# Kernel tuning notes

Hardware: AMD Instinct MI355X
Metric: run time of the kernel (lower is better)

## Reference

```python
import jax, jax.numpy as jnp
import numpy as np

N_NODES = 50000
N_EDGES = 600000
D_IN = 128
DIM = 128
N_REL = 3
N_LAYERS = 2


def setup_inputs() -> dict:
    key = jax.random.key(0)
    ks = jax.random.split(key, 10)
    s = 1.0 / np.sqrt(DIM)
    x = jax.random.normal(ks[0], (N_NODES, D_IN), dtype=jnp.float32)
    edge_index = jax.random.randint(ks[1], (2, N_EDGES), 0, N_NODES)
    edge_type = jax.random.randint(ks[2], (N_EDGES,), 0, N_REL)
    edge_weight = jax.random.uniform(ks[3], (N_EDGES,), dtype=jnp.float32)
    # stacked per-layer parameters (layer dims are uniform since D_IN == DIM)
    w_rel = jax.random.normal(ks[4], (N_LAYERS, N_REL, DIM, DIM), dtype=jnp.float32) * s
    w_root = jax.random.normal(ks[5], (N_LAYERS, DIM, DIM), dtype=jnp.float32) * s
    b_conv = jnp.zeros((N_LAYERS, DIM), dtype=jnp.float32)
    w_skip = jax.random.normal(ks[6], (N_LAYERS, D_IN, DIM), dtype=jnp.float32) * s
    b_skip = jnp.zeros((N_LAYERS, DIM), dtype=jnp.float32)
    return {"x": x, "edge_index": edge_index, "edge_type": edge_type,
            "edge_weight": edge_weight, "w_rel": w_rel, "w_root": w_root,
            "b_conv": b_conv, "w_skip": w_skip, "b_skip": b_skip}


def reference(x, edge_index, edge_type, edge_weight, w_rel, w_root, b_conv, w_skip, b_skip):
    n = x.shape[0]
    src, dst = edge_index[0], edge_index[1]
    h = x
    for l in range(w_rel.shape[0]):  # small fixed layer loop (2)
        skip = x @ w_skip[l] + b_skip[l]                      # [N, dim]
        # per-relation transform of all nodes: [R, N, dim] (cheap GEMMs),
        # avoids materializing a per-edge [E, d, d] weight gather
        hr = jnp.einsum('nd,rde->rne', h, w_rel[l])
        msgs = hr[edge_type, src] * edge_weight[:, None]      # [E, dim] gather
        agg = jax.ops.segment_sum(msgs, dst, num_segments=n)  # scatter-add
        h = agg + h @ w_root[l] + b_conv[l] + skip            # conv + skip residual
    return h
```

## Files before the change

kernel.cpp:

```cpp
#include <hip/hip_runtime.h>


#define DIM 128

typedef short short8 __attribute__((ext_vector_type(8)));
typedef float f32x4 __attribute__((ext_vector_type(4)));

__device__ __forceinline__ unsigned short f2bf(float f) {
    unsigned u = __float_as_uint(f);
    unsigned r = (u + 0x7FFFu + ((u >> 16) & 1u)) >> 16;
    return (unsigned short)r;
}
__device__ __forceinline__ float bflo(unsigned p) { return __uint_as_float(p << 16); }
__device__ __forceinline__ float bfhi(unsigned p) { return __uint_as_float(p & 0xFFFF0000u); }

__global__ void zero_kernel(int4* __restrict__ p, int n4) {
    int i = blockIdx.x * 256 + threadIdx.x;
    if (i < n4) p[i] = make_int4(0, 0, 0, 0);
}

#define K2_CONVB 2048
#define K2_PREPB 256
#define K2_CNTB  512

__device__ void conv_body(const float* __restrict__ in, unsigned short* __restrict__ ob,
                          int n8, int bid) {
    for (int i = bid * 256 + threadIdx.x; i < n8; i += K2_CONVB * 256) {
        const float4* ip = reinterpret_cast<const float4*>(in) + (size_t)i * 2;
        float4 v0 = ip[0], v1 = ip[1];
        uint4 o;
        o.x = (unsigned)f2bf(v0.x) | ((unsigned)f2bf(v0.y) << 16);
        o.y = (unsigned)f2bf(v0.z) | ((unsigned)f2bf(v0.w) << 16);
        o.z = (unsigned)f2bf(v1.x) | ((unsigned)f2bf(v1.y) << 16);
        o.w = (unsigned)f2bf(v1.z) | ((unsigned)f2bf(v1.w) << 16);
        reinterpret_cast<uint4*>(ob)[i] = o;
    }
}

__device__ void prep_body(const float* __restrict__ w_rel, const float* __restrict__ w_root,
                          const float* __restrict__ w_skip, unsigned short* __restrict__ WTf,
                          int bid) {
    for (int i = bid * 256 + threadIdx.x; i < 2 * 5 * DIM * DIM; i += K2_PREPB * 256) {
        int j    = i & 7;
        int lane = (i >> 3) & 63;
        int ks   = (i >> 9) & 3;
        int n    = (i >> 11) & 7;
        int s    = (i >> 14) % 5;
        int l    = i / (5 * DIM * DIM);
        int col = n * 16 + (lane & 15);
        int k   = ks * 32 + (lane >> 4) * 8 + j;
        float v;
        if (s < 3)       v = w_rel[(((size_t)l * 3 + s) * DIM + k) * DIM + col];
        else if (s == 3) {
            v = w_root[((size_t)l * DIM + k) * DIM + col];
            if (l == 0) v += w_skip[((size_t)k) * DIM + col];
        } else           v = w_skip[((size_t)l * DIM + k) * DIM + col];
        WTf[i] = f2bf(v);
    }
}

__device__ void count_body(const int* __restrict__ dst, int* __restrict__ counts,
                           unsigned short* __restrict__ rank, int E, int bid) {
    for (int i = bid * 256 + threadIdx.x; i < E; i += K2_CNTB * 256) {
        int r = atomicAdd(&counts[dst[i]], 1);
        rank[i] = (unsigned short)r;
    }
}

__global__ __launch_bounds__(256) void fat_prep(
    const float* __restrict__ x, unsigned short* __restrict__ xb, int n8,
    const float* __restrict__ w_rel, const float* __restrict__ w_root,
    const float* __restrict__ w_skip, unsigned short* __restrict__ WTf,
    const int* __restrict__ dst, int* __restrict__ counts,
    unsigned short* __restrict__ rank, int E) {
    int b = blockIdx.x;
    if (b < K2_CONVB)                 conv_body(x, xb, n8, b);
    else if (b < K2_CONVB + K2_PREPB) prep_body(w_rel, w_root, w_skip, WTf, b - K2_CONVB);
    else                              count_body(dst, counts, rank, E, b - K2_CONVB - K2_PREPB);
}

__global__ void bsum_kernel(const int* __restrict__ counts, int* __restrict__ bsums, int n) {
    int t = threadIdx.x;
    int i = blockIdx.x * 256 + t;
    int v = (i < n) ? counts[i] : 0;
    for (int d = 32; d; d >>= 1) v += __shfl_down(v, d);
    __shared__ int ws[4];
    if ((t & 63) == 0) ws[t >> 6] = v;
    __syncthreads();
    if (t == 0) bsums[blockIdx.x] = ws[0] + ws[1] + ws[2] + ws[3];
}

__global__ void bscan_kernel(const int* __restrict__ bsums, int* __restrict__ bpre, int nblk) {
    __shared__ int s[256];
    int t = threadIdx.x;
    int v = (t < nblk) ? bsums[t] : 0;
    s[t] = v;
    __syncthreads();
    for (int d = 1; d < 256; d <<= 1) {
        int u = (t >= d) ? s[t - d] : 0;
        __syncthreads();
        s[t] += u;
        __syncthreads();
    }
    bpre[t] = s[t] - v;
}

__global__ void scan_final(const int* __restrict__ counts, const int* __restrict__ bpre,
                           int* __restrict__ offsets, int n, int E) {
    __shared__ int s[256];
    int t = threadIdx.x;
    int i = blockIdx.x * 256 + t;
    int v = (i < n) ? counts[i] : 0;
    s[t] = v;
    __syncthreads();
    for (int d = 1; d < 256; d <<= 1) {
        int u = (t >= d) ? s[t - d] : 0;
        __syncthreads();
        s[t] += u;
        __syncthreads();
    }
    int ex = s[t] - v + bpre[blockIdx.x];
    if (i < n) offsets[i] = ex;
    if (i == 0) offsets[n] = E;
}

template<bool HAS_SKIP>
__device__ void gemm_body(
    int bid,
    const unsigned short* __restrict__ Ab, const unsigned short* __restrict__ Xb,
    const unsigned short* __restrict__ WTf,
    const float* __restrict__ bconv, const float* __restrict__ bskip,
    unsigned short* __restrict__ hr, void* __restrict__ outp, int M) {
    constexpr int NF = HAS_SKIP ? 40 : 32;
    __shared__ unsigned short stile[4][32][136];
    int t = threadIdx.x, lane = t & 63, wid = t >> 6;
    int lrow = lane & 15, lhi = lane >> 4;
    int r0 = bid * 128 + wid * 32;

    short8 af[2][4];
    #pragma unroll
    for (int rg = 0; rg < 2; ++rg) {
        int r = r0 + rg * 16 + lrow;
        const unsigned short* ap = Ab + (size_t)(r < M ? r : 0) * DIM + lhi * 8;
        #pragma unroll
        for (int ks = 0; ks < 4; ++ks)
            af[rg][ks] = *reinterpret_cast<const short8*>(ap + ks * 32);
    }
    short8 xf[2][4];
    f32x4 acc34[2][8];

    auto flush = [&](unsigned short* gbase) {
        #pragma unroll
        for (int j = 0; j < 8; ++j) {
            int lr = j * 4 + lhi;
            int lc = lrow * 8;
            int gr = r0 + lr;
            if (gr < M)
                *reinterpret_cast<uint4*>(gbase + (size_t)gr * DIM + lc) =
                    *reinterpret_cast<const uint4*>(&stile[wid][lr][lc]);
        }
    };

    short8 b0[4], b1[4];
    auto loadB = [&](int fi, short8* bb) {
        const unsigned short* p = WTf + ((size_t)fi * 4 * 64 + lane) * 8;
        #pragma unroll
        for (int ks = 0; ks < 4; ++ks)
            bb[ks] = *reinterpret_cast<const short8*>(p + ks * 512);
    };
    loadB(0, b0);
    #pragma unroll
    for (int fi = 0; fi < NF; ++fi) {
        short8* bc = (fi & 1) ? b1 : b0;
        short8* bn = (fi & 1) ? b0 : b1;
        if (fi + 1 < NF) loadB(fi + 1, bn);
        const int slot = fi >> 3, n = fi & 7;
        const int col = n * 16 + lrow;
        if (HAS_SKIP && slot == 3 && n == 0) {
            #pragma unroll
            for (int rg = 0; rg < 2; ++rg) {
                int r = r0 + rg * 16 + lrow;
                const unsigned short* xp = Xb + (size_t)(r < M ? r : 0) * DIM + lhi * 8;
                #pragma unroll
                for (int ks = 0; ks < 4; ++ks)
                    xf[rg][ks] = *reinterpret_cast<const short8*>(xp + ks * 32);
            }
        }
        if (slot < 3) {
            f32x4 a0 = {0.f, 0.f, 0.f, 0.f}, a1 = {0.f, 0.f, 0.f, 0.f};
            #pragma unroll
            for (int ks = 0; ks < 4; ++ks) {
                a0 = __builtin_amdgcn_mfma_f32_16x16x32_bf16(af[0][ks], bc[ks], a0, 0, 0, 0);
                a1 = __builtin_amdgcn_mfma_f32_16x16x32_bf16(af[1][ks], bc[ks], a1, 0, 0, 0);
            }
            #pragma unroll
            for (int rg = 0; rg < 2; ++rg) {
                f32x4& aa = rg ? a1 : a0;
                #pragma unroll
                for (int i2 = 0; i2 < 4; ++i2)
                    stile[wid][rg * 16 + lhi * 4 + i2][col] = f2bf(aa[i2]);
            }
            if (n == 7) flush(hr + (size_t)slot * M * DIM);
        } else if (!HAS_SKIP) {
            f32x4 a0 = {0.f, 0.f, 0.f, 0.f}, a1 = {0.f, 0.f, 0.f, 0.f};
            #pragma unroll
            for (int ks = 0; ks < 4; ++ks) {
                a0 = __builtin_amdgcn_mfma_f32_16x16x32_bf16(af[0][ks], bc[ks], a0, 0, 0, 0);
                a1 = __builtin_amdgcn_mfma_f32_16x16x32_bf16(af[1][ks], bc[ks], a1, 0, 0, 0);
            }
            float bb = bconv[col] + bskip[col];
            #pragma unroll
            for (int rg = 0; rg < 2; ++rg) {
                f32x4& aa = rg ? a1 : a0;
                #pragma unroll
                for (int i2 = 0; i2 < 4; ++i2)
                    stile[wid][rg * 16 + lhi * 4 + i2][col] = f2bf(aa[i2] + bb);
            }
            if (n == 7) flush((unsigned short*)outp);
        } else if (slot == 3) {
            f32x4 z = {0.f, 0.f, 0.f, 0.f};
            acc34[0][n] = z; acc34[1][n] = z;
            #pragma unroll
            for (int ks = 0; ks < 4; ++ks) {
                acc34[0][n] = __builtin_amdgcn_mfma_f32_16x16x32_bf16(af[0][ks], bc[ks], acc34[0][n], 0, 0, 0);
                acc34[1][n] = __builtin_amdgcn_mfma_f32_16x16x32_bf16(af[1][ks], bc[ks], acc34[1][n], 0, 0, 0);
            }
        } else {
            #pragma unroll
            for (int ks = 0; ks < 4; ++ks) {
                acc34[0][n] = __builtin_amdgcn_mfma_f32_16x16x32_bf16(xf[0][ks], bc[ks], acc34[0][n], 0, 0, 0);
                acc34[1][n] = __builtin_amdgcn_mfma_f32_16x16x32_bf16(xf[1][ks], bc[ks], acc34[1][n], 0, 0, 0);
            }
            float bb = bconv[col] + bskip[col];
            float* op = (float*)outp;
            #pragma unroll
            for (int rg = 0; rg < 2; ++rg) {
                #pragma unroll
                for (int i2 = 0; i2 < 4; ++i2) {
                    int r = r0 + rg * 16 + lhi * 4 + i2;
                    if (r < M) op[(size_t)r * DIM + col] = acc34[rg][n][i2] + bb;
                }
            }
        }
    }
}

#define K6_SCTB 512

__device__ void scatter_body(const int* __restrict__ src, const int* __restrict__ dst,
                             const int* __restrict__ etype, const float* __restrict__ ew,
                             const int* __restrict__ offsets,
                             const unsigned short* __restrict__ rank,
                             unsigned* __restrict__ csr, int E, int bid) {
    for (int i = bid * 256 + threadIdx.x; i < E; i += K6_SCTB * 256) {
        int d = dst[i];
        int p = offsets[d] + rank[i];
        unsigned wq = (unsigned)__float2uint_rn(ew[i] * 16383.0f);
        csr[p] = (unsigned)src[i] | ((unsigned)etype[i] << 16) | (wq << 18);
    }
}

__global__ __launch_bounds__(256) void gemm0_scatter(
    const unsigned short* __restrict__ Ab, const unsigned short* __restrict__ WTf,
    const float* __restrict__ bconv, const float* __restrict__ bskip,
    unsigned short* __restrict__ hr, unsigned short* __restrict__ h1, int M, int GB,
    const int* __restrict__ src, const int* __restrict__ dst,
    const int* __restrict__ etype, const float* __restrict__ ew,
    const int* __restrict__ offsets, const unsigned short* __restrict__ rank,
    unsigned* __restrict__ csr, int E) {
    int b = blockIdx.x;
    if (b < GB) gemm_body<false>(b, Ab, nullptr, WTf, bconv, bskip, hr, h1, M);
    else        scatter_body(src, dst, etype, ew, offsets, rank, csr, E, b - GB);
}

__global__ __launch_bounds__(256) void gemm1_kernel(
    const unsigned short* __restrict__ Ab, const unsigned short* __restrict__ Xb,
    const unsigned short* __restrict__ WTf,
    const float* __restrict__ bconv, const float* __restrict__ bskip,
    unsigned short* __restrict__ hr, float* __restrict__ outp, int M) {
    gemm_body<true>(blockIdx.x, Ab, Xb, WTf, bconv, bskip, hr, outp, M);
}

template<bool BF16IO>
__global__ __launch_bounds__(256) void agg_kernel(
    const unsigned short* __restrict__ hr, const unsigned* __restrict__ csr,
    const int* __restrict__ offsets, float* __restrict__ outf,
    unsigned short* __restrict__ outb, int N) {
    int t = threadIdx.x;
    int lane = t & 63;
    int v = blockIdx.x * 4 + (t >> 6);
    if (v >= N) return;
    int g = lane >> 4;
    int l16 = lane & 15;
    int beg = offsets[v], end = offsets[v + 1];

    float acc[8] = {0.f, 0.f, 0.f, 0.f, 0.f, 0.f, 0.f, 0.f};
    int i = beg + g;
    bool valid = i < end;
    unsigned st = valid ? csr[i] : 0u;
    while (__any(valid)) {
        int ni = i + 4;
        bool nv = ni < end;
        unsigned nst = nv ? csr[ni] : 0u;
        if (valid) {
            int srcn = st & 0xFFFF;
            int rel  = (st >> 16) & 3;
            float w  = (float)(st >> 18) * (1.0f / 16383.0f);
            const unsigned short* row = hr + ((size_t)rel * N + srcn) * DIM + l16 * 8;
            uint4 pv = *reinterpret_cast<const uint4*>(row);
            acc[0] += w * bflo(pv.x); acc[1] += w * bfhi(pv.x);
            acc[2] += w * bflo(pv.y); acc[3] += w * bfhi(pv.y);
            acc[4] += w * bflo(pv.z); acc[5] += w * bfhi(pv.z);
            acc[6] += w * bflo(pv.w); acc[7] += w * bfhi(pv.w);
        }
        i = ni; st = nst; valid = nv;
    }
    #pragma unroll
    for (int j = 0; j < 8; ++j) {
        acc[j] += __shfl_xor(acc[j], 16);
        acc[j] += __shfl_xor(acc[j], 32);
    }
    if (g == 0) {
        if (BF16IO) {
            unsigned short* op = outb + (size_t)v * DIM + l16 * 8;
            uint4 cur = *reinterpret_cast<const uint4*>(op);
            float r0 = bflo(cur.x) + acc[0], r1 = bfhi(cur.x) + acc[1];
            float r2 = bflo(cur.y) + acc[2], r3 = bfhi(cur.y) + acc[3];
            float r4 = bflo(cur.z) + acc[4], r5 = bfhi(cur.z) + acc[5];
            float r6 = bflo(cur.w) + acc[6], r7 = bfhi(cur.w) + acc[7];
            uint4 o;
            o.x = (unsigned)f2bf(r0) | ((unsigned)f2bf(r1) << 16);
            o.y = (unsigned)f2bf(r2) | ((unsigned)f2bf(r3) << 16);
            o.z = (unsigned)f2bf(r4) | ((unsigned)f2bf(r5) << 16);
            o.w = (unsigned)f2bf(r6) | ((unsigned)f2bf(r7) << 16);
            *reinterpret_cast<uint4*>(op) = o;
        } else {
            float* op = outf + (size_t)v * DIM + l16 * 8;
            float4 c0 = *reinterpret_cast<float4*>(op);
            float4 c1 = *reinterpret_cast<float4*>(op + 4);
            c0.x += acc[0]; c0.y += acc[1]; c0.z += acc[2]; c0.w += acc[3];
            c1.x += acc[4]; c1.y += acc[5]; c1.z += acc[6]; c1.w += acc[7];
            *reinterpret_cast<float4*>(op) = c0;
            *reinterpret_cast<float4*>(op + 4) = c1;
        }
    }
}

extern "C" void kernel_launch(void* const* d_in, const int* in_sizes, int n_in,
                              void* d_out, int out_size, void* d_ws, size_t ws_size,
                              hipStream_t stream) {
    const float* x       = (const float*)d_in[0];
    const int*   eidx    = (const int*)d_in[1];
    const int*   etype   = (const int*)d_in[2];
    const float* ew      = (const float*)d_in[3];
    const float* w_rel   = (const float*)d_in[4];
    const float* w_root  = (const float*)d_in[5];
    const float* b_conv  = (const float*)d_in[6];
    const float* w_skip  = (const float*)d_in[7];
    const float* b_skip  = (const float*)d_in[8];

    const int N = in_sizes[0] / DIM;
    const int E = in_sizes[3];
    const int* src = eidx;
    const int* dst = eidx + E;
    const int nblk = (N + 255) / 256;

    char* w = (char*)d_ws;
    unsigned short* WTf  = (unsigned short*)w;  w += (size_t)2 * 5 * DIM * DIM * 2;
    unsigned short* xb   = (unsigned short*)w;  w += (size_t)N * DIM * 2;
    unsigned short* hr   = (unsigned short*)w;  w += (size_t)3 * N * DIM * 2;
    unsigned short* h1   = (unsigned short*)w;  w += (size_t)N * DIM * 2;
    int* counts          = (int*)w;             w += (size_t)N * 4;
    int* offsets         = (int*)w;             w += (size_t)(N + 4) * 4;
    int* bsums           = (int*)w;             w += (size_t)256 * 4;
    int* bpre            = (int*)w;             w += (size_t)256 * 4;
    unsigned short* rank = (unsigned short*)w;  w += (size_t)E * 2;
    unsigned* csr        = (unsigned*)w;        w += (size_t)E * 4;

    float* out = (float*)d_out;

    const int n8 = N * DIM / 8;
    zero_kernel<<<(N / 4 + 255) / 256, 256, 0, stream>>>((int4*)counts, N / 4);
    fat_prep<<<K2_CONVB + K2_PREPB + K2_CNTB, 256, 0, stream>>>(
        x, xb, n8, w_rel, w_root, w_skip, WTf, dst, counts, rank, E);
    bsum_kernel<<<nblk, 256, 0, stream>>>(counts, bsums, N);
    bscan_kernel<<<1, 256, 0, stream>>>(bsums, bpre, nblk);
    scan_final<<<nblk, 256, 0, stream>>>(counts, bpre, offsets, N, E);

    int GB = (N + 127) / 128;
    int ablocks = (N + 3) / 4;
    gemm0_scatter<<<GB + K6_SCTB, 256, 0, stream>>>(
        xb, WTf, b_conv, b_skip, hr, h1, N, GB,
        src, dst, etype, ew, offsets, rank, csr, E);
    agg_kernel<true><<<ablocks, 256, 0, stream>>>(hr, csr, offsets, nullptr, h1, N);
    gemm1_kernel<<<GB, 256, 0, stream>>>(h1, xb, WTf + (size_t)5 * DIM * DIM,
                                         b_conv + DIM, b_skip + DIM, hr, out, N);
    agg_kernel<false><<<ablocks, 256, 0, stream>>>(hr, csr, offsets, out, nullptr, N);
}
```

Measured before the change: 159.4 us.

## Privatize degree counters into eight partitions to reduce atomic contention

The per-destination degree counting now spreads its atomics across eight copies of the count array, selected by block index, and each thread issues four independent atomics per iteration for more memory-level parallelism. The scan kernels sum the eight partitions and write per-partition starting positions, which the scatter uses with the edge's partition, recovered from its index, to place CSR entries. This aims to cut same-address atomic contention in the counting phase. In exchange it adds eight times the counter zeroing, extra reads in both scans, and a larger pos0 lookup table in the scatter.

```diff
diff --git a/kernel.cpp b/kernel.cpp
--- a/kernel.cpp
+++ b/kernel.cpp
@@ -59,11 +59,24 @@
     }
 }
 
-__device__ void count_body(const int* __restrict__ dst, int* __restrict__ counts,
-                           unsigned short* __restrict__ rank, int E, int bid) {
-    for (int i = bid * 256 + threadIdx.x; i < E; i += K2_CNTB * 256) {
-        int r = atomicAdd(&counts[dst[i]], 1);
-        rank[i] = (unsigned short)r;
+__device__ void count_body(const int* __restrict__ dst, int* __restrict__ counts8,
+                           unsigned short* __restrict__ rank, int E, int N, int bid) {
+    int* cp = counts8 + (size_t)(bid & 7) * N;
+    int t = threadIdx.x;
+    for (int base = bid * 1024; base < E; base += K2_CNTB * 1024) {
+        int i0 = base + t, i1 = i0 + 256, i2 = i0 + 512, i3 = i0 + 768;
+        int d0 = (i0 < E) ? dst[i0] : -1;
+        int d1 = (i1 < E) ? dst[i1] : -1;
+        int d2 = (i2 < E) ? dst[i2] : -1;
+        int d3 = (i3 < E) ? dst[i3] : -1;
+        int r0 = (d0 >= 0) ? atomicAdd(&cp[d0], 1) : 0;
+        int r1 = (d1 >= 0) ? atomicAdd(&cp[d1], 1) : 0;
+        int r2 = (d2 >= 0) ? atomicAdd(&cp[d2], 1) : 0;
+        int r3 = (d3 >= 0) ? atomicAdd(&cp[d3], 1) : 0;
+        if (d0 >= 0) rank[i0] = (unsigned short)r0;
+        if (d1 >= 0) rank[i1] = (unsigned short)r1;
+        if (d2 >= 0) rank[i2] = (unsigned short)r2;
+        if (d3 >= 0) rank[i3] = (unsigned short)r3;
     }
 }
 
@@ -71,18 +84,22 @@
     const float* __restrict__ x, unsigned short* __restrict__ xb, int n8,
     const float* __restrict__ w_rel, const float* __restrict__ w_root,
     const float* __restrict__ w_skip, unsigned short* __restrict__ WTf,
-    const int* __restrict__ dst, int* __restrict__ counts,
-    unsigned short* __restrict__ rank, int E) {
+    const int* __restrict__ dst, int* __restrict__ counts8,
+    unsigned short* __restrict__ rank, int E, int N) {
     int b = blockIdx.x;
     if (b < K2_CONVB)                 conv_body(x, xb, n8, b);
     else if (b < K2_CONVB + K2_PREPB) prep_body(w_rel, w_root, w_skip, WTf, b - K2_CONVB);
-    else                              count_body(dst, counts, rank, E, b - K2_CONVB - K2_PREPB);
-}
-
-__global__ void bsum_kernel(const int* __restrict__ counts, int* __restrict__ bsums, int n) {
+    else                              count_body(dst, counts8, rank, E, N, b - K2_CONVB - K2_PREPB);
+}
+
+__global__ void bsum_kernel(const int* __restrict__ counts8, int* __restrict__ bsums, int n) {
     int t = threadIdx.x;
     int i = blockIdx.x * 256 + t;
-    int v = (i < n) ? counts[i] : 0;
+    int v = 0;
+    if (i < n) {
+        #pragma unroll
+        for (int p = 0; p < 8; ++p) v += counts8[(size_t)p * n + i];
+    }
     for (int d = 32; d; d >>= 1) v += __shfl_down(v, d);
     __shared__ int ws[4];
     if ((t & 63) == 0) ws[t >> 6] = v;
@@ -105,12 +122,18 @@
     bpre[t] = s[t] - v;
 }
 
-__global__ void scan_final(const int* __restrict__ counts, const int* __restrict__ bpre,
-                           int* __restrict__ offsets, int n, int E) {
+__global__ void scan_final(const int* __restrict__ counts8, const int* __restrict__ bpre,
+                           int* __restrict__ offsets, int* __restrict__ pos0,
+                           int n, int E) {
     __shared__ int s[256];
     int t = threadIdx.x;
     int i = blockIdx.x * 256 + t;
-    int v = (i < n) ? counts[i] : 0;
+    int c[8];
+    int v = 0;
+    if (i < n) {
+        #pragma unroll
+        for (int p = 0; p < 8; ++p) { c[p] = counts8[(size_t)p * n + i]; v += c[p]; }
+    }
     s[t] = v;
     __syncthreads();
     for (int d = 1; d < 256; d <<= 1) {
@@ -120,7 +143,12 @@
         __syncthreads();
     }
     int ex = s[t] - v + bpre[blockIdx.x];
-    if (i < n) offsets[i] = ex;
+    if (i < n) {
+        offsets[i] = ex;
+        int run = ex;
+        #pragma unroll
+        for (int p = 0; p < 8; ++p) { pos0[(size_t)p * n + i] = run; run += c[p]; }
+    }
     if (i == 0) offsets[n] = E;
 }
 
@@ -249,12 +277,13 @@
 
 __device__ void scatter_body(const int* __restrict__ src, const int* __restrict__ dst,
                              const int* __restrict__ etype, const float* __restrict__ ew,
-                             const int* __restrict__ offsets,
+                             const int* __restrict__ pos0,
                              const unsigned short* __restrict__ rank,
-                             unsigned* __restrict__ csr, int E, int bid) {
+                             unsigned* __restrict__ csr, int E, int N, int bid) {
     for (int i = bid * 256 + threadIdx.x; i < E; i += K6_SCTB * 256) {
         int d = dst[i];
-        int p = offsets[d] + rank[i];
+        int part = (i >> 10) & 7;
+        int p = pos0[(size_t)part * N + d] + rank[i];
         unsigned wq = (unsigned)__float2uint_rn(ew[i] * 16383.0f);
         csr[p] = (unsigned)src[i] | ((unsigned)etype[i] << 16) | (wq << 18);
     }
@@ -266,11 +295,11 @@
     unsigned short* __restrict__ hr, unsigned short* __restrict__ h1, int M, int GB,
     const int* __restrict__ src, const int* __restrict__ dst,
     const int* __restrict__ etype, const float* __restrict__ ew,
-    const int* __restrict__ offsets, const unsigned short* __restrict__ rank,
+    const int* __restrict__ pos0, const unsigned short* __restrict__ rank,
     unsigned* __restrict__ csr, int E) {
     int b = blockIdx.x;
     if (b < GB) gemm_body<false>(b, Ab, nullptr, WTf, bconv, bskip, hr, h1, M);
-    else        scatter_body(src, dst, etype, ew, offsets, rank, csr, E, b - GB);
+    else        scatter_body(src, dst, etype, ew, pos0, rank, csr, E, M, b - GB);
 }
 
 __global__ __launch_bounds__(256) void gemm1_kernel(
@@ -370,7 +399,8 @@
     unsigned short* xb   = (unsigned short*)w;  w += (size_t)N * DIM * 2;
     unsigned short* hr   = (unsigned short*)w;  w += (size_t)3 * N * DIM * 2;
     unsigned short* h1   = (unsigned short*)w;  w += (size_t)N * DIM * 2;
-    int* counts          = (int*)w;             w += (size_t)N * 4;
+    int* counts8         = (int*)w;             w += (size_t)8 * N * 4;
+    int* pos0            = (int*)w;             w += (size_t)8 * N * 4;
     int* offsets         = (int*)w;             w += (size_t)(N + 4) * 4;
     int* bsums           = (int*)w;             w += (size_t)256 * 4;
     int* bpre            = (int*)w;             w += (size_t)256 * 4;
@@ -380,18 +410,18 @@
     float* out = (float*)d_out;
 
     const int n8 = N * DIM / 8;
-    zero_kernel<<<(N / 4 + 255) / 256, 256, 0, stream>>>((int4*)counts, N / 4);
+    zero_kernel<<<(8 * N / 4 + 255) / 256, 256, 0, stream>>>((int4*)counts8, 8 * N / 4);
     fat_prep<<<K2_CONVB + K2_PREPB + K2_CNTB, 256, 0, stream>>>(
-        x, xb, n8, w_rel, w_root, w_skip, WTf, dst, counts, rank, E);
-    bsum_kernel<<<nblk, 256, 0, stream>>>(counts, bsums, N);
+        x, xb, n8, w_rel, w_root, w_skip, WTf, dst, counts8, rank, E, N);
+    bsum_kernel<<<nblk, 256, 0, stream>>>(counts8, bsums, N);
     bscan_kernel<<<1, 256, 0, stream>>>(bsums, bpre, nblk);
-    scan_final<<<nblk, 256, 0, stream>>>(counts, bpre, offsets, N, E);
+    scan_final<<<nblk, 256, 0, stream>>>(counts8, bpre, offsets, pos0, N, E);
 
     int GB = (N + 127) / 128;
     int ablocks = (N + 3) / 4;
     gemm0_scatter<<<GB + K6_SCTB, 256, 0, stream>>>(
         xb, WTf, b_conv, b_skip, hr, h1, N, GB,
-        src, dst, etype, ew, offsets, rank, csr, E);
+        src, dst, etype, ew, pos0, rank, csr, E);
     agg_kernel<true><<<ablocks, 256, 0, stream>>>(hr, csr, offsets, nullptr, h1, N);
     gemm1_kernel<<<GB, 256, 0, stream>>>(h1, xb, WTf + (size_t)5 * DIM * DIM,
                                          b_conv + DIM, b_skip + DIM, hr, out, N);
```

Result: no change. 159.8 us (+0.2%).

## Pad degree counters, batch count atomics, dual-issue gathers in aggregation

Applied to the files above, without the earlier changes.

Degree counters are padded to a 64-byte stride so atomics on nearby destination nodes no longer share cache lines. The count loop now issues four independent atomics per thread per iteration, and its blocks are launched first so this atomic-heavy work starts early. The aggregation kernel keeps two edge gathers in flight per lane group, prefetching the CSR entries ahead. The padding makes the counts buffer and the zeroing pass sixteen times larger, and the scan kernels now read counters with a strided access pattern.

```diff
diff --git a/kernel.cpp b/kernel.cpp
--- a/kernel.cpp
+++ b/kernel.cpp
@@ -2,6 +2,7 @@
 
 
 #define DIM 128
+#define CSTRIDE 16
 
 typedef short short8 __attribute__((ext_vector_type(8)));
 typedef float f32x4 __attribute__((ext_vector_type(4)));
@@ -19,9 +20,9 @@
     if (i < n4) p[i] = make_int4(0, 0, 0, 0);
 }
 
+#define K2_CNTB  512
+#define K2_PREPB 256
 #define K2_CONVB 2048
-#define K2_PREPB 256
-#define K2_CNTB  512
 
 __device__ void conv_body(const float* __restrict__ in, unsigned short* __restrict__ ob,
                           int n8, int bid) {
@@ -61,9 +62,21 @@
 
 __device__ void count_body(const int* __restrict__ dst, int* __restrict__ counts,
                            unsigned short* __restrict__ rank, int E, int bid) {
-    for (int i = bid * 256 + threadIdx.x; i < E; i += K2_CNTB * 256) {
-        int r = atomicAdd(&counts[dst[i]], 1);
-        rank[i] = (unsigned short)r;
+    int t = threadIdx.x;
+    for (int base = bid * 1024; base < E; base += K2_CNTB * 1024) {
+        int i0 = base + t, i1 = i0 + 256, i2 = i0 + 512, i3 = i0 + 768;
+        int d0 = (i0 < E) ? dst[i0] : -1;
+        int d1 = (i1 < E) ? dst[i1] : -1;
+        int d2 = (i2 < E) ? dst[i2] : -1;
+        int d3 = (i3 < E) ? dst[i3] : -1;
+        int r0 = (d0 >= 0) ? atomicAdd(&counts[(size_t)d0 * CSTRIDE], 1) : 0;
+        int r1 = (d1 >= 0) ? atomicAdd(&counts[(size_t)d1 * CSTRIDE], 1) : 0;
+        int r2 = (d2 >= 0) ? atomicAdd(&counts[(size_t)d2 * CSTRIDE], 1) : 0;
+        int r3 = (d3 >= 0) ? atomicAdd(&counts[(size_t)d3 * CSTRIDE], 1) : 0;
+        if (d0 >= 0) rank[i0] = (unsigned short)r0;
+        if (d1 >= 0) rank[i1] = (unsigned short)r1;
+        if (d2 >= 0) rank[i2] = (unsigned short)r2;
+        if (d3 >= 0) rank[i3] = (unsigned short)r3;
     }
 }
 
@@ -74,15 +87,15 @@
     const int* __restrict__ dst, int* __restrict__ counts,
     unsigned short* __restrict__ rank, int E) {
     int b = blockIdx.x;
-    if (b < K2_CONVB)                 conv_body(x, xb, n8, b);
-    else if (b < K2_CONVB + K2_PREPB) prep_body(w_rel, w_root, w_skip, WTf, b - K2_CONVB);
-    else                              count_body(dst, counts, rank, E, b - K2_CONVB - K2_PREPB);
+    if (b < K2_CNTB)                 count_body(dst, counts, rank, E, b);
+    else if (b < K2_CNTB + K2_PREPB) prep_body(w_rel, w_root, w_skip, WTf, b - K2_CNTB);
+    else                             conv_body(x, xb, n8, b - K2_CNTB - K2_PREPB);
 }
 
 __global__ void bsum_kernel(const int* __restrict__ counts, int* __restrict__ bsums, int n) {
     int t = threadIdx.x;
     int i = blockIdx.x * 256 + t;
-    int v = (i < n) ? counts[i] : 0;
+    int v = (i < n) ? counts[(size_t)i * CSTRIDE] : 0;
     for (int d = 32; d; d >>= 1) v += __shfl_down(v, d);
     __shared__ int ws[4];
     if ((t & 63) == 0) ws[t >> 6] = v;
@@ -110,7 +123,7 @@
     __shared__ int s[256];
     int t = threadIdx.x;
     int i = blockIdx.x * 256 + t;
-    int v = (i < n) ? counts[i] : 0;
+    int v = (i < n) ? counts[(size_t)i * CSTRIDE] : 0;
     s[t] = v;
     __syncthreads();
     for (int d = 1; d < 256; d <<= 1) {
@@ -295,25 +308,39 @@
     int beg = offsets[v], end = offsets[v + 1];
 
     float acc[8] = {0.f, 0.f, 0.f, 0.f, 0.f, 0.f, 0.f, 0.f};
-    int i = beg + g;
-    bool valid = i < end;
-    unsigned st = valid ? csr[i] : 0u;
-    while (__any(valid)) {
-        int ni = i + 4;
-        bool nv = ni < end;
-        unsigned nst = nv ? csr[ni] : 0u;
-        if (valid) {
-            int srcn = st & 0xFFFF;
-            int rel  = (st >> 16) & 3;
-            float w  = (float)(st >> 18) * (1.0f / 16383.0f);
-            const unsigned short* row = hr + ((size_t)rel * N + srcn) * DIM + l16 * 8;
-            uint4 pv = *reinterpret_cast<const uint4*>(row);
-            acc[0] += w * bflo(pv.x); acc[1] += w * bfhi(pv.x);
-            acc[2] += w * bflo(pv.y); acc[3] += w * bfhi(pv.y);
-            acc[4] += w * bflo(pv.z); acc[5] += w * bfhi(pv.z);
-            acc[6] += w * bflo(pv.w); acc[7] += w * bfhi(pv.w);
-        }
-        i = ni; st = nst; valid = nv;
+    int iA = beg + g, iB = iA + 4;
+    bool vA = iA < end, vB = iB < end;
+    unsigned sA = vA ? csr[iA] : 0u;
+    unsigned sB = vB ? csr[iB] : 0u;
+    while (__any(vA)) {
+        uint4 pA = make_uint4(0, 0, 0, 0), pB = make_uint4(0, 0, 0, 0);
+        if (vA) {
+            const unsigned short* row = hr + ((size_t)((sA >> 16) & 3) * N + (sA & 0xFFFF)) * DIM + l16 * 8;
+            pA = *reinterpret_cast<const uint4*>(row);
+        }
+        if (vB) {
+            const unsigned short* row = hr + ((size_t)((sB >> 16) & 3) * N + (sB & 0xFFFF)) * DIM + l16 * 8;
+            pB = *reinterpret_cast<const uint4*>(row);
+        }
+        int nA = iA + 8, nB = iB + 8;
+        bool nvA = nA < end, nvB = nB < end;
+        unsigned nsA = nvA ? csr[nA] : 0u;
+        unsigned nsB = nvB ? csr[nB] : 0u;
+        if (vA) {
+            float w = (float)(sA >> 18) * (1.0f / 16383.0f);
+            acc[0] += w * bflo(pA.x); acc[1] += w * bfhi(pA.x);
+            acc[2] += w * bflo(pA.y); acc[3] += w * bfhi(pA.y);
+            acc[4] += w * bflo(pA.z); acc[5] += w * bfhi(pA.z);
+            acc[6] += w * bflo(pA.w); acc[7] += w * bfhi(pA.w);
+        }
+        if (vB) {
+            float w = (float)(sB >> 18) * (1.0f / 16383.0f);
+            acc[0] += w * bflo(pB.x); acc[1] += w * bfhi(pB.x);
+            acc[2] += w * bflo(pB.y); acc[3] += w * bfhi(pB.y);
+            acc[4] += w * bflo(pB.z); acc[5] += w * bfhi(pB.z);
+            acc[6] += w * bflo(pB.w); acc[7] += w * bfhi(pB.w);
+        }
+        iA = nA; iB = nB; sA = nsA; sB = nsB; vA = nvA; vB = nvB;
     }
     #pragma unroll
     for (int j = 0; j < 8; ++j) {
@@ -370,7 +397,7 @@
     unsigned short* xb   = (unsigned short*)w;  w += (size_t)N * DIM * 2;
     unsigned short* hr   = (unsigned short*)w;  w += (size_t)3 * N * DIM * 2;
     unsigned short* h1   = (unsigned short*)w;  w += (size_t)N * DIM * 2;
-    int* counts          = (int*)w;             w += (size_t)N * 4;
+    int* counts          = (int*)w;             w += (size_t)N * CSTRIDE * 4;
     int* offsets         = (int*)w;             w += (size_t)(N + 4) * 4;
     int* bsums           = (int*)w;             w += (size_t)256 * 4;
     int* bpre            = (int*)w;             w += (size_t)256 * 4;
@@ -380,8 +407,9 @@
     float* out = (float*)d_out;
 
     const int n8 = N * DIM / 8;
-    zero_kernel<<<(N / 4 + 255) / 256, 256, 0, stream>>>((int4*)counts, N / 4);
-    fat_prep<<<K2_CONVB + K2_PREPB + K2_CNTB, 256, 0, stream>>>(
+    const int zc = N * CSTRIDE / 4;
+    zero_kernel<<<(zc + 255) / 256, 256, 0, stream>>>((int4*)counts, zc);
+    fat_prep<<<K2_CNTB + K2_PREPB + K2_CONVB, 256, 0, stream>>>(
         x, xb, n8, w_rel, w_root, w_skip, WTf, dst, counts, rank, E);
     bsum_kernel<<<nblk, 256, 0, stream>>>(counts, bsums, N);
     bscan_kernel<<<1, 256, 0, stream>>>(bsums, bpre, nblk);
```

Result: faster. 152.0 us (-4.6%).
